# Kernel tuning notes

Hardware: AMD Instinct MI355X
Metric: run time of the kernel (lower is better)

## Reference

```python
import jax, jax.numpy as jnp
import numpy as np

SPATIAL_SHAPES = np.array([[100, 100], [50, 50], [25, 25], [13, 13]], dtype=np.int32)
EMBED, NH, NL, NP = 256, 8, 4, 4
HD = EMBED // NH  # 32


def setup_inputs() -> dict:
    key = jax.random.key(0)
    ks = jax.random.split(key, 12)
    bs, nq = 4, 4000
    nv = int((SPATIAL_SHAPES[:, 0] * SPATIAL_SHAPES[:, 1]).sum())  # 13294
    s_lin = 1.0 / np.sqrt(EMBED)  # xavier-ish scale
    s_small = 0.02                # offsets/weights heads start near init
    return {
        "query": jax.random.normal(ks[0], (bs, nq, EMBED), jnp.float32),
        "value": jax.random.normal(ks[1], (bs, nv, EMBED), jnp.float32),
        "reference_points": jax.random.uniform(ks[2], (bs, nq, NL, 2), jnp.float32),
        "spatial_shapes": jnp.asarray(SPATIAL_SHAPES),
        "W_off": jax.random.normal(ks[3], (EMBED, NH * NL * NP * 2), jnp.float32) * s_small,
        "b_off": jax.random.normal(ks[4], (NH * NL * NP * 2,), jnp.float32) * s_small,
        "W_attn": jax.random.normal(ks[5], (EMBED, NH * NL * NP), jnp.float32) * s_small,
        "b_attn": jax.random.normal(ks[6], (NH * NL * NP,), jnp.float32) * s_small,
        "W_val": jax.random.normal(ks[7], (EMBED, EMBED), jnp.float32) * s_lin,
        "b_val": jnp.zeros((EMBED,), jnp.float32),
        "W_out": jax.random.normal(ks[8], (EMBED, EMBED), jnp.float32) * s_lin,
        "b_out": jnp.zeros((EMBED,), jnp.float32),
    }


def _bilinear_sample(val_l, H, W, x, y):
    """grid_sample(mode=bilinear, padding=zeros, align_corners=False) equivalent.
    val_l: [bs, nh, H*W, hd]; x, y: [bs, nh, nq, np] pixel-space coords.
    Returns [bs, nh, nq, np, hd]."""
    x0 = jnp.floor(x)
    y0 = jnp.floor(y)
    bs, nh, nq, npts = x.shape
    out = 0.0
    for dx, dy in ((0, 0), (1, 0), (0, 1), (1, 1)):
        xi = x0 + dx
        yi = y0 + dy
        w = (1.0 - jnp.abs(x - xi)) * (1.0 - jnp.abs(y - yi))
        valid = (xi >= 0) & (xi < W) & (yi >= 0) & (yi < H)
        idx = (jnp.clip(yi, 0, H - 1) * W + jnp.clip(xi, 0, W - 1)).astype(jnp.int32)
        g = jnp.take_along_axis(val_l, idx.reshape(bs, nh, nq * npts, 1), axis=2)
        g = g.reshape(bs, nh, nq, npts, -1)
        out = out + g * (w * valid.astype(w.dtype))[..., None]
    return out


def reference(query, value, reference_points, spatial_shapes,
              W_off, b_off, W_attn, b_attn, W_val, b_val, W_out, b_out):
    shapes = np.asarray(spatial_shapes)  # static level shapes
    bs, nq, _ = query.shape
    # value projection -> per-head layout [bs, nh, nv, hd]
    v = (value @ W_val + b_val).reshape(bs, -1, NH, HD).transpose(0, 2, 1, 3)
    # sampling offsets and attention weights from query
    off = (query @ W_off + b_off).reshape(bs, nq, NH, NL, NP, 2)
    attn = jax.nn.softmax((query @ W_attn + b_attn).reshape(bs, nq, NH, NL * NP), axis=-1)
    attn = attn.reshape(bs, nq, NH, NL, NP)
    # normalized sampling locations; normalizer = (W, H) per level
    normalizer = jnp.asarray(np.stack([shapes[:, 1], shapes[:, 0]], -1), jnp.float32)
    loc = reference_points[:, :, None, :, None, :] + off / normalizer[None, None, None, :, None, :]
    out = jnp.zeros((bs, NH, nq, HD), query.dtype)
    start = 0
    for l in range(NL):
        H, W = int(shapes[l, 0]), int(shapes[l, 1])
        val_l = v[:, :, start:start + H * W, :]
        # pixel coords with align_corners=False: p = loc*size - 0.5
        x = loc[:, :, :, l, :, 0].transpose(0, 2, 1, 3) * W - 0.5  # [bs,nh,nq,np]
        y = loc[:, :, :, l, :, 1].transpose(0, 2, 1, 3) * H - 0.5
        sampled = _bilinear_sample(val_l, H, W, x, y)  # [bs,nh,nq,np,hd]
        out = out + jnp.einsum('bhqpd,bqhp->bhqd', sampled, attn[:, :, :, l, :])
        start += H * W
    out = out.transpose(0, 2, 1, 3).reshape(bs, nq, EMBED)
    return out @ W_out + b_out
```

## Files before the change

kernel.cpp:

```cpp
#include <hip/hip_runtime.h>
#include <hip/hip_bf16.h>

#define EMBED 256
#define NH 8
#define NL 4
#define NP 4
#define HD 32
#define BS 4
#define NQ 4000
#define NV 13294

using f32x4   = __attribute__((ext_vector_type(4))) float;
using bf16x8  = __attribute__((ext_vector_type(8))) short;

__device__ __forceinline__ float bf2f_lo(unsigned u) {
    union { unsigned u; float f; } x; x.u = u << 16; return x.f;
}
__device__ __forceinline__ float bf2f_hi(unsigned u) {
    union { unsigned u; float f; } x; x.u = u & 0xffff0000u; return x.f;
}
__device__ __forceinline__ unsigned short f2bf(float f) {
    union { float f; unsigned u; } x; x.f = f;
    unsigned u = x.u;
    return (unsigned short)((u + 0x7fffu + ((u >> 16) & 1u)) >> 16);
}

__global__ __launch_bounds__(256) void msda_prep_k(
    const float* __restrict__ value, const float* __restrict__ query,
    const float* __restrict__ W_val, const float* __restrict__ W_out,
    const float* __restrict__ W_off, const float* __restrict__ W_attn,
    const float* __restrict__ b_off, const float* __restrict__ b_attn,
    unsigned short* __restrict__ value_bf, unsigned short* __restrict__ query_bf,
    unsigned short* __restrict__ Wt_val, unsigned short* __restrict__ Wt_out,
    unsigned short* __restrict__ Wt_qa, float* __restrict__ b_qa)
{
    const int bid = blockIdx.x, tid = threadIdx.x;
    if (bid < 13294) {
        int i = bid * 256 + tid;
        float4 v = ((const float4*)value)[i];
        uint2 o = { f2bf(v.x) | ((unsigned)f2bf(v.y) << 16),
                    f2bf(v.z) | ((unsigned)f2bf(v.w) << 16) };
        ((uint2*)value_bf)[i] = o;
    } else if (bid < 17294) {
        int i = (bid - 13294) * 256 + tid;
        float4 v = ((const float4*)query)[i];
        uint2 o = { f2bf(v.x) | ((unsigned)f2bf(v.y) << 16),
                    f2bf(v.z) | ((unsigned)f2bf(v.w) << 16) };
        ((uint2*)query_bf)[i] = o;
    } else {
        int i = (bid - 17294) * 256 + tid;
        if (i < 384) b_qa[i] = (i < 256) ? b_off[i] : b_attn[i - 256];
        if (i < 65536) {
            int r = i >> 8, c = i & 255;
            Wt_val[c * 256 + r] = f2bf(W_val[i]);
        } else if (i < 131072) {
            int j = i - 65536, r = j >> 8, c = j & 255;
            Wt_out[c * 256 + r] = f2bf(W_out[j]);
        } else if (i < 229376) {
            int j = i - 131072;
            int n = j >> 8, k = j & 255;
            float v = (n < 256) ? W_off[k * 256 + n] : W_attn[k * 128 + (n - 256)];
            Wt_qa[j] = f2bf(v);
        }
    }
}

template<int EPI>
__global__ __launch_bounds__(256, 2) void msda_gemm_k(
    const unsigned short* __restrict__ A,
    const unsigned short* __restrict__ Bt,
    const float* __restrict__ bias,
    void* __restrict__ out,
    int M, int N)
{
    constexpr int K = 256;
    __shared__ __align__(16) unsigned short Bs[128][256];
    const int m0 = blockIdx.x * 128, n0 = blockIdx.y * 128;
    const int tid  = threadIdx.x;
    const int w    = tid >> 6;
    const int lane = tid & 63;
    const int quad = lane >> 4;
    const int l16  = lane & 15;
    const int wm   = (w & 1) * 64, wn = (w >> 1) * 64;

    {
        const int r0 = tid >> 5;
        const int ch = tid & 31;
#pragma unroll
        for (int j = 0; j < 16; j++) {
            int row = j * 8 + r0;
            uint4 v = *(const uint4*)(Bt + (size_t)(n0 + row) * K + ch * 8);
            int g = ch ^ (row & 7);
            *(uint4*)((char*)&Bs[row][0] + g * 16) = v;
        }
    }

    const unsigned short* aptr[4];
#pragma unroll
    for (int mi = 0; mi < 4; mi++) {
        int r = min(m0 + wm + mi * 16 + l16, M - 1);
        aptr[mi] = A + (size_t)r * K + quad * 8;
    }

    f32x4 acc[4][4];
#pragma unroll
    for (int a = 0; a < 4; a++)
#pragma unroll
        for (int b = 0; b < 4; b++) acc[a][b] = (f32x4){0.f, 0.f, 0.f, 0.f};

    __syncthreads();

    bf16x8 areg[3][4];
#pragma unroll
    for (int mi = 0; mi < 4; mi++) areg[0][mi] = *(const bf16x8*)(aptr[mi]);
#pragma unroll
    for (int mi = 0; mi < 4; mi++) areg[1][mi] = *(const bf16x8*)(aptr[mi] + 32);

#pragma unroll
    for (int c = 0; c < 8; c++) {
        if (c + 2 < 8) {
#pragma unroll
            for (int mi = 0; mi < 4; mi++)
                areg[(c + 2) % 3][mi] = *(const bf16x8*)(aptr[mi] + (c + 2) * 32);
        }
        bf16x8 bfr[4];
#pragma unroll
        for (int ni = 0; ni < 4; ni++) {
            int row = wn + ni * 16 + l16;
            int g = (c * 4 + quad) ^ (row & 7);
            bfr[ni] = *(const bf16x8*)((const char*)&Bs[row][0] + g * 16);
        }
        const int cb = c % 3;
#pragma unroll
        for (int mi = 0; mi < 4; mi++)
#pragma unroll
            for (int ni = 0; ni < 4; ni++)
                acc[mi][ni] = __builtin_amdgcn_mfma_f32_16x16x32_bf16(areg[cb][mi], bfr[ni], acc[mi][ni], 0, 0, 0);
    }

#pragma unroll
    for (int ni = 0; ni < 4; ni++) {
        int cc = n0 + wn + ni * 16 + l16;
        float bvv = bias[cc];
#pragma unroll
        for (int mi = 0; mi < 4; mi++) {
#pragma unroll
            for (int r = 0; r < 4; r++) {
                int m = m0 + wm + mi * 16 + quad * 4 + r;
                if (m >= M) continue;
                float val = acc[mi][ni][r] + bvv;
                if (EPI == 0) {
                    ((unsigned short*)out)[(size_t)m * N + cc] = f2bf(val);
                } else {
                    ((float*)out)[(size_t)m * N + cc] = val;
                }
            }
        }
    }
}

__global__ __launch_bounds__(256) void msda_sampler_k(
    const float* __restrict__ refpts,
    const float* __restrict__ oa_buf,
    const unsigned short* __restrict__ v_buf,
    unsigned short* __restrict__ t_out)
{
    __shared__ float4 wtab[1088];
    __shared__ int4   itab[1088];

    const int tid = threadIdx.x;
    const int q0  = blockIdx.x * 8;

    const int HWs[4]    = {100, 50, 25, 13};
    const int starts[4] = {0, 10000, 12500, 13125};

#pragma unroll
    for (int it = 0; it < 4; it++) {
        int s  = it * 256 + tid;
        int i  = s & 15;
        int g  = s >> 4;
        int ql = g >> 3, h = g & 7;
        int l  = i >> 2, p = i & 3;
        int q  = q0 + ql;
        const float* oa = oa_buf + (size_t)q * 384;

        float logit = oa[256 + h * 16 + i];
        float m = logit;
#pragma unroll
        for (int off = 1; off < 16; off <<= 1) m = fmaxf(m, __shfl_xor(m, off, 64));
        float e = __expf(logit - m);
        float sum = e;
#pragma unroll
        for (int off = 1; off < 16; off <<= 1) sum += __shfl_xor(sum, off, 64);
        float a = e / sum;

        int Wl = HWs[l];
        float fW = (float)Wl;
        float rx = refpts[q * 8 + l * 2], ry = refpts[q * 8 + l * 2 + 1];
        float offx = oa[h * 32 + l * 8 + p * 2];
        float offy = oa[h * 32 + l * 8 + p * 2 + 1];
        float x = rx * fW + offx - 0.5f;
        float y = ry * fW + offy - 0.5f;
        float xf = floorf(x), yf = floorf(y);
        float fx = x - xf, fy = y - yf;
        int x0 = (int)xf, y0 = (int)yf;
        int x1 = x0 + 1, y1 = y0 + 1;
        float wx0 = (x0 >= 0 && x0 < Wl) ? (1.f - fx) : 0.f;
        float wx1 = (x1 >= 0 && x1 < Wl) ? fx : 0.f;
        float wy0 = (y0 >= 0 && y0 < Wl) ? (1.f - fy) : 0.f;
        float wy1 = (y1 >= 0 && y1 < Wl) ? fy : 0.f;
        int x0c = min(max(x0, 0), Wl - 1), x1c = min(max(x1, 0), Wl - 1);
        int y0c = min(max(y0, 0), Wl - 1), y1c = min(max(y1, 0), Wl - 1);
        int r0 = starts[l] + y0c * Wl, r1 = starts[l] + y1c * Wl;
        int ti = g * 17 + i;
        wtab[ti] = make_float4(wx0 * wy0 * a, wx1 * wy0 * a, wx0 * wy1 * a, wx1 * wy1 * a);
        itab[ti] = make_int4(r0 + x0c, r0 + x1c, r1 + x0c, r1 + x1c);
    }
    __syncthreads();

    const int ql = tid >> 5, h = (tid >> 2) & 7, dg = tid & 3;
    const int q = q0 + ql;
    const int b = q / NQ;
    const char* base = (const char*)v_buf + (size_t)b * NV * 512;
    const unsigned coff = (unsigned)h * 64 + (unsigned)dg * 16;
    const int gi = (ql * 8 + h) * 17;

    float a0 = 0.f, a1 = 0.f, a2 = 0.f, a3 = 0.f;
    float a4 = 0.f, a5 = 0.f, a6 = 0.f, a7 = 0.f;
#pragma unroll
    for (int lp = 0; lp < 16; lp++) {
        float4 wv = wtab[gi + lp];
        int4   ix = itab[gi + lp];
        uint4 s0 = *(const uint4*)(base + (((unsigned)ix.x << 9) + coff));
        uint4 s1 = *(const uint4*)(base + (((unsigned)ix.y << 9) + coff));
        uint4 s2 = *(const uint4*)(base + (((unsigned)ix.z << 9) + coff));
        uint4 s3 = *(const uint4*)(base + (((unsigned)ix.w << 9) + coff));
        a0 += wv.x * bf2f_lo(s0.x); a1 += wv.x * bf2f_hi(s0.x);
        a2 += wv.x * bf2f_lo(s0.y); a3 += wv.x * bf2f_hi(s0.y);
        a4 += wv.x * bf2f_lo(s0.z); a5 += wv.x * bf2f_hi(s0.z);
        a6 += wv.x * bf2f_lo(s0.w); a7 += wv.x * bf2f_hi(s0.w);
        a0 += wv.y * bf2f_lo(s1.x); a1 += wv.y * bf2f_hi(s1.x);
        a2 += wv.y * bf2f_lo(s1.y); a3 += wv.y * bf2f_hi(s1.y);
        a4 += wv.y * bf2f_lo(s1.z); a5 += wv.y * bf2f_hi(s1.z);
        a6 += wv.y * bf2f_lo(s1.w); a7 += wv.y * bf2f_hi(s1.w);
        a0 += wv.z * bf2f_lo(s2.x); a1 += wv.z * bf2f_hi(s2.x);
        a2 += wv.z * bf2f_lo(s2.y); a3 += wv.z * bf2f_hi(s2.y);
        a4 += wv.z * bf2f_lo(s2.z); a5 += wv.z * bf2f_hi(s2.z);
        a6 += wv.z * bf2f_lo(s2.w); a7 += wv.z * bf2f_hi(s2.w);
        a0 += wv.w * bf2f_lo(s3.x); a1 += wv.w * bf2f_hi(s3.x);
        a2 += wv.w * bf2f_lo(s3.y); a3 += wv.w * bf2f_hi(s3.y);
        a4 += wv.w * bf2f_lo(s3.z); a5 += wv.w * bf2f_hi(s3.z);
        a6 += wv.w * bf2f_lo(s3.w); a7 += wv.w * bf2f_hi(s3.w);
    }
    uint4 o = { (unsigned)f2bf(a0) | ((unsigned)f2bf(a1) << 16),
                (unsigned)f2bf(a2) | ((unsigned)f2bf(a3) << 16),
                (unsigned)f2bf(a4) | ((unsigned)f2bf(a5) << 16),
                (unsigned)f2bf(a6) | ((unsigned)f2bf(a7) << 16) };
    *(uint4*)(t_out + (size_t)q * 256 + h * 32 + dg * 8) = o;
}

extern "C" void kernel_launch(void* const* d_in, const int* in_sizes, int n_in,
                              void* d_out, int out_size, void* d_ws, size_t ws_size,
                              hipStream_t stream) {
    const float* query  = (const float*)d_in[0];
    const float* value  = (const float*)d_in[1];
    const float* refpts = (const float*)d_in[2];
    const float* W_off  = (const float*)d_in[4];
    const float* b_off  = (const float*)d_in[5];
    const float* W_attn = (const float*)d_in[6];
    const float* b_attn = (const float*)d_in[7];
    const float* W_val  = (const float*)d_in[8];
    const float* b_val  = (const float*)d_in[9];
    const float* W_out  = (const float*)d_in[10];
    const float* b_out  = (const float*)d_in[11];

    char* wsp = (char*)d_ws;
    size_t o = 0;
    auto carve = [&](size_t bytes) -> void* {
        void* p = wsp + o; o += (bytes + 255) & ~(size_t)255; return p;
    };
    unsigned short* Wt_val = (unsigned short*)carve(256 * 256 * 2);
    unsigned short* Wt_out = (unsigned short*)carve(256 * 256 * 2);
    unsigned short* Wt_qa  = (unsigned short*)carve(384 * 256 * 2);
    float*          b_qa   = (float*)carve(384 * 4);
    unsigned short* v_buf  = (unsigned short*)carve((size_t)BS * NV * EMBED * 2);
    char* regX = (char*)carve((size_t)BS * NV * EMBED * 2);
    unsigned short* value_bf = (unsigned short*)regX;
    float*          oa_buf   = (float*)regX;
    char* regY = (char*)carve((size_t)BS * NQ * EMBED * 2);
    unsigned short* query_bf = (unsigned short*)regY;
    unsigned short* t_buf    = (unsigned short*)regY;

    msda_prep_k<<<18190, 256, 0, stream>>>(value, query, W_val, W_out, W_off, W_attn,
                                           b_off, b_attn, value_bf, query_bf,
                                           Wt_val, Wt_out, Wt_qa, b_qa);

    const int Mv = BS * NV;
    const int Mq = BS * NQ;
    msda_gemm_k<0><<<dim3((Mv + 127) / 128, 2), 256, 0, stream>>>(value_bf, Wt_val, b_val, v_buf, Mv, 256);
    msda_gemm_k<1><<<dim3(Mq / 128, 3), 256, 0, stream>>>(query_bf, Wt_qa, b_qa, oa_buf, Mq, 384);
    msda_sampler_k<<<Mq / 8, 256, 0, stream>>>(refpts, oa_buf, v_buf, t_buf);
    msda_gemm_k<1><<<dim3(Mq / 128, 2), 256, 0, stream>>>(t_buf, Wt_out, b_out, (float*)d_out, Mq, 256);
}
```

Measured before the change: 224.3 us.

## Fuse value and query GEMMs, head-major value layout, split sampler corners

The value-projection and query offset/attention GEMMs now run as one launch, and oa_buf gets its own workspace region so the two can run concurrently. The value-projection epilogue writes v_buf head-major ([b][h][s][32]), so each head's samples hit a compact 64-byte-row region. The sampler handles 4 queries per block with two threads per (head, d-group), each doing one x-corner, and combines them with a shuffle. The GEMM A-register prefetch depth grows from 2 to 3 chunks, raising register pressure and workspace use.

```diff
diff --git a/kernel.cpp b/kernel.cpp
--- a/kernel.cpp
+++ b/kernel.cpp
@@ -65,17 +65,15 @@
     }
 }
 
-template<int EPI>
-__global__ __launch_bounds__(256, 2) void msda_gemm_k(
+template<typename EpiF>
+__device__ __forceinline__ void gemm_core(
     const unsigned short* __restrict__ A,
     const unsigned short* __restrict__ Bt,
     const float* __restrict__ bias,
-    void* __restrict__ out,
-    int M, int N)
+    int M, int N, int m0, int n0, EpiF epi)
 {
     constexpr int K = 256;
     __shared__ __align__(16) unsigned short Bs[128][256];
-    const int m0 = blockIdx.x * 128, n0 = blockIdx.y * 128;
     const int tid  = threadIdx.x;
     const int w    = tid >> 6;
     const int lane = tid & 63;
@@ -108,20 +106,21 @@
 #pragma unroll
         for (int b = 0; b < 4; b++) acc[a][b] = (f32x4){0.f, 0.f, 0.f, 0.f};
 
+    bf16x8 areg[4][4];
+#pragma unroll
+    for (int c0 = 0; c0 < 3; c0++)
+#pragma unroll
+        for (int mi = 0; mi < 4; mi++)
+            areg[c0][mi] = *(const bf16x8*)(aptr[mi] + c0 * 32);
+
     __syncthreads();
 
-    bf16x8 areg[3][4];
-#pragma unroll
-    for (int mi = 0; mi < 4; mi++) areg[0][mi] = *(const bf16x8*)(aptr[mi]);
-#pragma unroll
-    for (int mi = 0; mi < 4; mi++) areg[1][mi] = *(const bf16x8*)(aptr[mi] + 32);
-
 #pragma unroll
     for (int c = 0; c < 8; c++) {
-        if (c + 2 < 8) {
+        if (c + 3 < 8) {
 #pragma unroll
             for (int mi = 0; mi < 4; mi++)
-                areg[(c + 2) % 3][mi] = *(const bf16x8*)(aptr[mi] + (c + 2) * 32);
+                areg[(c + 3) & 3][mi] = *(const bf16x8*)(aptr[mi] + (c + 3) * 32);
         }
         bf16x8 bfr[4];
 #pragma unroll
@@ -130,7 +129,7 @@
             int g = (c * 4 + quad) ^ (row & 7);
             bfr[ni] = *(const bf16x8*)((const char*)&Bs[row][0] + g * 16);
         }
-        const int cb = c % 3;
+        const int cb = c & 3;
 #pragma unroll
         for (int mi = 0; mi < 4; mi++)
 #pragma unroll
@@ -148,15 +147,52 @@
             for (int r = 0; r < 4; r++) {
                 int m = m0 + wm + mi * 16 + quad * 4 + r;
                 if (m >= M) continue;
-                float val = acc[mi][ni][r] + bvv;
-                if (EPI == 0) {
-                    ((unsigned short*)out)[(size_t)m * N + cc] = f2bf(val);
-                } else {
-                    ((float*)out)[(size_t)m * N + cc] = val;
-                }
+                epi(m, cc, acc[mi][ni][r] + bvv);
             }
         }
     }
+}
+
+__global__ __launch_bounds__(256, 2) void msda_gemm12_k(
+    const unsigned short* __restrict__ value_bf,
+    const unsigned short* __restrict__ query_bf,
+    const unsigned short* __restrict__ Wt_val,
+    const unsigned short* __restrict__ Wt_qa,
+    const float* __restrict__ b_val,
+    const float* __restrict__ b_qa,
+    unsigned short* __restrict__ v_buf,
+    float* __restrict__ oa_buf)
+{
+    const int bid = blockIdx.x;
+    if (bid < 832) {
+        const int m0 = (bid >> 1) * 128, n0 = (bid & 1) * 128;
+        gemm_core(value_bf, Wt_val, b_val, BS * NV, 256, m0, n0,
+            [&](int m, int cc, float val) {
+                int b = m / NV, s = m - b * NV;
+                int h = cc >> 5, d = cc & 31;
+                v_buf[(((size_t)(b * NH + h) * NV + s) << 5) + d] = f2bf(val);
+            });
+    } else {
+        const int j = bid - 832;
+        const int m0 = (j / 3) * 128, n0 = (j % 3) * 128;
+        gemm_core(query_bf, Wt_qa, b_qa, BS * NQ, 384, m0, n0,
+            [&](int m, int cc, float val) {
+                oa_buf[(size_t)m * 384 + cc] = val;
+            });
+    }
+}
+
+__global__ __launch_bounds__(256, 2) void msda_gemm3_k(
+    const unsigned short* __restrict__ t_buf,
+    const unsigned short* __restrict__ Wt_out,
+    const float* __restrict__ b_out,
+    float* __restrict__ out)
+{
+    const int m0 = blockIdx.x * 128, n0 = blockIdx.y * 128;
+    gemm_core(t_buf, Wt_out, b_out, BS * NQ, 256, m0, n0,
+        [&](int m, int cc, float val) {
+            out[(size_t)m * 256 + cc] = val;
+        });
 }
 
 __global__ __launch_bounds__(256) void msda_sampler_k(
@@ -165,17 +201,17 @@
     const unsigned short* __restrict__ v_buf,
     unsigned short* __restrict__ t_out)
 {
-    __shared__ float4 wtab[1088];
-    __shared__ int4   itab[1088];
+    __shared__ float4 wtab[544];
+    __shared__ int4   itab[544];
 
     const int tid = threadIdx.x;
-    const int q0  = blockIdx.x * 8;
+    const int q0  = blockIdx.x * 4;
 
     const int HWs[4]    = {100, 50, 25, 13};
     const int starts[4] = {0, 10000, 12500, 13125};
 
 #pragma unroll
-    for (int it = 0; it < 4; it++) {
+    for (int it = 0; it < 2; it++) {
         int s  = it * 256 + tid;
         int i  = s & 15;
         int g  = s >> 4;
@@ -211,18 +247,18 @@
         float wy1 = (y1 >= 0 && y1 < Wl) ? fy : 0.f;
         int x0c = min(max(x0, 0), Wl - 1), x1c = min(max(x1, 0), Wl - 1);
         int y0c = min(max(y0, 0), Wl - 1), y1c = min(max(y1, 0), Wl - 1);
-        int r0 = starts[l] + y0c * Wl, r1 = starts[l] + y1c * Wl;
         int ti = g * 17 + i;
-        wtab[ti] = make_float4(wx0 * wy0 * a, wx1 * wy0 * a, wx0 * wy1 * a, wx1 * wy1 * a);
-        itab[ti] = make_int4(r0 + x0c, r0 + x1c, r1 + x0c, r1 + x1c);
+        wtab[ti] = make_float4(wx0 * a, wx1 * a, wy0, wy1);
+        itab[ti] = make_int4(x0c * 64, x1c * 64,
+                             (starts[l] + y0c * Wl) * 64,
+                             (starts[l] + y1c * Wl) * 64);
     }
     __syncthreads();
 
-    const int ql = tid >> 5, h = (tid >> 2) & 7, dg = tid & 3;
+    const int dg = tid & 3, xc = (tid >> 2) & 1, h = (tid >> 3) & 7, ql = tid >> 6;
     const int q = q0 + ql;
     const int b = q / NQ;
-    const char* base = (const char*)v_buf + (size_t)b * NV * 512;
-    const unsigned coff = (unsigned)h * 64 + (unsigned)dg * 16;
+    const char* base = (const char*)v_buf + ((size_t)(b * NH + h) * NV) * 64 + dg * 16;
     const int gi = (ql * 8 + h) * 17;
 
     float a0 = 0.f, a1 = 0.f, a2 = 0.f, a3 = 0.f;
@@ -231,32 +267,31 @@
     for (int lp = 0; lp < 16; lp++) {
         float4 wv = wtab[gi + lp];
         int4   ix = itab[gi + lp];
-        uint4 s0 = *(const uint4*)(base + (((unsigned)ix.x << 9) + coff));
-        uint4 s1 = *(const uint4*)(base + (((unsigned)ix.y << 9) + coff));
-        uint4 s2 = *(const uint4*)(base + (((unsigned)ix.z << 9) + coff));
-        uint4 s3 = *(const uint4*)(base + (((unsigned)ix.w << 9) + coff));
-        a0 += wv.x * bf2f_lo(s0.x); a1 += wv.x * bf2f_hi(s0.x);
-        a2 += wv.x * bf2f_lo(s0.y); a3 += wv.x * bf2f_hi(s0.y);
-        a4 += wv.x * bf2f_lo(s0.z); a5 += wv.x * bf2f_hi(s0.z);
-        a6 += wv.x * bf2f_lo(s0.w); a7 += wv.x * bf2f_hi(s0.w);
-        a0 += wv.y * bf2f_lo(s1.x); a1 += wv.y * bf2f_hi(s1.x);
-        a2 += wv.y * bf2f_lo(s1.y); a3 += wv.y * bf2f_hi(s1.y);
-        a4 += wv.y * bf2f_lo(s1.z); a5 += wv.y * bf2f_hi(s1.z);
-        a6 += wv.y * bf2f_lo(s1.w); a7 += wv.y * bf2f_hi(s1.w);
-        a0 += wv.z * bf2f_lo(s2.x); a1 += wv.z * bf2f_hi(s2.x);
-        a2 += wv.z * bf2f_lo(s2.y); a3 += wv.z * bf2f_hi(s2.y);
-        a4 += wv.z * bf2f_lo(s2.z); a5 += wv.z * bf2f_hi(s2.z);
-        a6 += wv.z * bf2f_lo(s2.w); a7 += wv.z * bf2f_hi(s2.w);
-        a0 += wv.w * bf2f_lo(s3.x); a1 += wv.w * bf2f_hi(s3.x);
-        a2 += wv.w * bf2f_lo(s3.y); a3 += wv.w * bf2f_hi(s3.y);
-        a4 += wv.w * bf2f_lo(s3.z); a5 += wv.w * bf2f_hi(s3.z);
-        a6 += wv.w * bf2f_lo(s3.w); a7 += wv.w * bf2f_hi(s3.w);
-    }
-    uint4 o = { (unsigned)f2bf(a0) | ((unsigned)f2bf(a1) << 16),
-                (unsigned)f2bf(a2) | ((unsigned)f2bf(a3) << 16),
-                (unsigned)f2bf(a4) | ((unsigned)f2bf(a5) << 16),
-                (unsigned)f2bf(a6) | ((unsigned)f2bf(a7) << 16) };
-    *(uint4*)(t_out + (size_t)q * 256 + h * 32 + dg * 8) = o;
+        int   xb = xc ? ix.y : ix.x;
+        float wx = xc ? wv.y : wv.x;
+        uint4 s0 = *(const uint4*)(base + (ix.z + xb));
+        uint4 s1 = *(const uint4*)(base + (ix.w + xb));
+        float w0 = wx * wv.z, w1 = wx * wv.w;
+        a0 += w0 * bf2f_lo(s0.x); a1 += w0 * bf2f_hi(s0.x);
+        a2 += w0 * bf2f_lo(s0.y); a3 += w0 * bf2f_hi(s0.y);
+        a4 += w0 * bf2f_lo(s0.z); a5 += w0 * bf2f_hi(s0.z);
+        a6 += w0 * bf2f_lo(s0.w); a7 += w0 * bf2f_hi(s0.w);
+        a0 += w1 * bf2f_lo(s1.x); a1 += w1 * bf2f_hi(s1.x);
+        a2 += w1 * bf2f_lo(s1.y); a3 += w1 * bf2f_hi(s1.y);
+        a4 += w1 * bf2f_lo(s1.z); a5 += w1 * bf2f_hi(s1.z);
+        a6 += w1 * bf2f_lo(s1.w); a7 += w1 * bf2f_hi(s1.w);
+    }
+    a0 += __shfl_xor(a0, 4, 64); a1 += __shfl_xor(a1, 4, 64);
+    a2 += __shfl_xor(a2, 4, 64); a3 += __shfl_xor(a3, 4, 64);
+    a4 += __shfl_xor(a4, 4, 64); a5 += __shfl_xor(a5, 4, 64);
+    a6 += __shfl_xor(a6, 4, 64); a7 += __shfl_xor(a7, 4, 64);
+    if (xc == 0) {
+        uint4 o = { (unsigned)f2bf(a0) | ((unsigned)f2bf(a1) << 16),
+                    (unsigned)f2bf(a2) | ((unsigned)f2bf(a3) << 16),
+                    (unsigned)f2bf(a4) | ((unsigned)f2bf(a5) << 16),
+                    (unsigned)f2bf(a6) | ((unsigned)f2bf(a7) << 16) };
+        *(uint4*)(t_out + (size_t)q * 256 + h * 32 + dg * 8) = o;
+    }
 }
 
 extern "C" void kernel_launch(void* const* d_in, const int* in_sizes, int n_in,
@@ -295,10 +330,11 @@
                                            b_off, b_attn, value_bf, query_bf,
                                            Wt_val, Wt_out, Wt_qa, b_qa);
 
-    const int Mv = BS * NV;
-    const int Mq = BS * NQ;
-    msda_gemm_k<0><<<dim3((Mv + 127) / 128, 2), 256, 0, stream>>>(value_bf, Wt_val, b_val, v_buf, Mv, 256);
-    msda_gemm_k<1><<<dim3(Mq / 128, 3), 256, 0, stream>>>(query_bf, Wt_qa, b_qa, oa_buf, Mq, 384);
-    msda_sampler_k<<<Mq / 8, 256, 0, stream>>>(refpts, oa_buf, v_buf, t_buf);
-    msda_gemm_k<1><<<dim3(Mq / 128, 2), 256, 0, stream>>>(t_buf, Wt_out, b_out, (float*)d_out, Mq, 256);
-}
+    (void)oa_buf;
+    float* oa_buf2 = (float*)carve((size_t)BS * NQ * 384 * 4);
+
+    msda_gemm12_k<<<1207, 256, 0, stream>>>(value_bf, query_bf, Wt_val, Wt_qa,
+                                            b_val, b_qa, v_buf, oa_buf2);
+    msda_sampler_k<<<BS * NQ / 4, 256, 0, stream>>>(refpts, oa_buf2, v_buf, t_buf);
+    msda_gemm3_k<<<dim3(BS * NQ / 128, 2), 256, 0, stream>>>(t_buf, Wt_out, b_out, (float*)d_out);
+}
```

Result: slower. 244.4 us (+8.9%).
